# Performance work log

Measured on AMD Instinct MI355X. Metric: run time of the kernel, lower is better.

Reference implementation:

```python
import jax, jax.numpy as jnp
import numpy as np

CH_IN, CH_OUT, KH, KW = 64, 128, 3, 3


def setup_inputs() -> dict:
    key = jax.random.key(0)
    k1, k2, k3 = jax.random.split(key, 3)
    x = jax.random.normal(k1, (16, CH_IN, 256, 256), dtype=jnp.float32)
    W_hat = jax.random.normal(k2, (CH_OUT, CH_IN * KH * KW), dtype=jnp.float32)
    M_hat = jax.random.normal(k3, (CH_OUT, CH_IN * KH * KW), dtype=jnp.float32)
    return {"x": x, "W_hat": W_hat, "M_hat": M_hat}


def reference(x, W_hat, M_hat):
    # NAC weight transform, then a standard same-padded conv (no bias).
    # Patch flattening order in the original (narrow(-1)/narrow(-2) then reshape)
    # matches (C_in, KH, KW) conv weight layout.
    W = jnp.tanh(W_hat) * jax.nn.sigmoid(M_hat)          # [C_out, C_in*KH*KW]
    W = W.reshape(CH_OUT, CH_IN, KH, KW)                  # OIHW
    out = jax.lax.conv_general_dilated(
        x, W,
        window_strides=(1, 1),
        padding=((KH // 2, KH // 2), (KW // 2, KW // 2)),
        dimension_numbers=("NCHW", "OIHW", "NCHW"),
    )
    return out
```

## Files before the change

kernel.cpp:

```cpp
#include <hip/hip_runtime.h>
#include <hip/hip_bf16.h>
#include <stdint.h>


#define CH_IN  64
#define CH_OUT 128
#define HW     256
#define NBATCH 16

typedef __attribute__((ext_vector_type(8))) short short8;
typedef __attribute__((ext_vector_type(4))) float f32x4;

static __device__ __forceinline__ uint32_t pack_bf16(float a, float b) {
    uint32_t ua = __builtin_bit_cast(uint32_t, a);
    uint32_t ub = __builtin_bit_cast(uint32_t, b);
    ua = (ua + 0x7FFFu + ((ua >> 16) & 1u)) >> 16;
    ub = (ub + 0x7FFFu + ((ub >> 16) & 1u));
    return (ua & 0xFFFFu) | (ub & 0xFFFF0000u);
}

__global__ void __launch_bounds__(256) nac_prep(const float* __restrict__ Wh,
                                                const float* __restrict__ Mh,
                                                uint32_t* __restrict__ Af) {
    int f = blockIdx.x * 256 + threadIdx.x;
    if (f >= 9 * 8 * 2 * 64) return;
    int lane = f & 63;
    int s    = (f >> 6) & 1;
    int ms   = (f >> 7) & 7;
    int t    = f >> 10;
    int co   = ms * 16 + (lane & 15);
    int ci0  = s * 32 + ((lane >> 4) << 3);

    uint32_t pk[4];
#pragma unroll
    for (int j2 = 0; j2 < 4; ++j2) {
        int ci = ci0 + 2 * j2;
        int k0 = ci * 9 + t;
        int k1 = k0 + 9;
        float w0 = tanhf(Wh[co * 576 + k0]);
        float m0 = Mh[co * 576 + k0];
        float w1 = tanhf(Wh[co * 576 + k1]);
        float m1 = Mh[co * 576 + k1];
        float v0 = w0 * (1.0f / (1.0f + expf(-m0)));
        float v1 = w1 * (1.0f / (1.0f + expf(-m1)));
        pk[j2] = pack_bf16(v0, v1);
    }
    int fragidx = ((t * 8 + ms) * 2 + s) * 64 + lane;
    reinterpret_cast<uint4*>(Af)[fragidx] = make_uint4(pk[0], pk[1], pk[2], pk[3]);
}

__global__ void __launch_bounds__(256) nac_conv(const float* __restrict__ x,
                                                const uint32_t* __restrict__ Af,
                                                float* __restrict__ out) {
    __shared__ uint32_t xl[8 * 272 * 4];

    unsigned bid = blockIdx.x;
    unsigned idx = (bid & 7u) * 1024u + (bid >> 3);
    int ht = idx & 127;
    int wt = (idx >> 7) & 3;
    int n  = idx >> 9;
    int h0 = ht * 2;
    int w0 = wt * 64;

    int tid = threadIdx.x;

    const float* xn = x + (size_t)n * CH_IN * HW * HW;
    for (int it = 0; it < 9; ++it) {
        int task = tid + it * 256;
        if (task < 2176) {
            int r   = task / 544;
            int rem = task - r * 544;
            int pg  = rem / 68;
            int c   = rem - pg * 68;
            int hrow = h0 - 1 + r;
            int w    = w0 - 1 + c;
            float v[8];
            if ((unsigned)hrow < 256u && (unsigned)w < 256u) {
                const float* p = xn + ((size_t)(pg * 8) * HW + hrow) * HW + w;
#pragma unroll
                for (int e = 0; e < 8; ++e) v[e] = p[(size_t)e * HW * HW];
            } else {
#pragma unroll
                for (int e = 0; e < 8; ++e) v[e] = 0.0f;
            }
            uint4 wd;
            wd.x = pack_bf16(v[0], v[1]);
            wd.y = pack_bf16(v[2], v[3]);
            wd.z = pack_bf16(v[4], v[5]);
            wd.w = pack_bf16(v[6], v[7]);
            *reinterpret_cast<uint4*>(&xl[(pg * 272 + r * 68 + c) * 4]) = wd;
        }
    }
    __syncthreads();

    int lane = tid & 63;
    int wv   = tid >> 6;
    int wm   = wv >> 1;
    int wn   = wv & 1;
    int row4 = lane >> 4;
    int col  = lane & 15;

    f32x4 acc[4][4];
#pragma unroll
    for (int mi = 0; mi < 4; ++mi)
#pragma unroll
        for (int ni = 0; ni < 4; ++ni)
            acc[mi][ni] = (f32x4){0.f, 0.f, 0.f, 0.f};

    const short8* Afr = reinterpret_cast<const short8*>(Af);

    for (int t = 0; t < 9; ++t) {
        int kh = t / 3, kw = t % 3;
        short8 a[2][4];
#pragma unroll
        for (int s = 0; s < 2; ++s)
#pragma unroll
            for (int mi = 0; mi < 4; ++mi)
                a[s][mi] = Afr[((t * 8 + (wm * 4 + mi)) * 2 + s) * 64 + lane];

#pragma unroll
        for (int s = 0; s < 2; ++s) {
            short8 b[4];
#pragma unroll
            for (int ni = 0; ni < 4; ++ni) {
                int pg = s * 4 + row4;
                int pp = (wn + kh) * 68 + ni * 16 + col + kw;
                b[ni] = *reinterpret_cast<const short8*>(&xl[(pg * 272 + pp) * 4]);
            }
#pragma unroll
            for (int mi = 0; mi < 4; ++mi)
#pragma unroll
                for (int ni = 0; ni < 4; ++ni)
                    acc[mi][ni] = __builtin_amdgcn_mfma_f32_16x16x32_bf16(
                        a[s][mi], b[ni], acc[mi][ni], 0, 0, 0);
        }
    }

#pragma unroll
    for (int mi = 0; mi < 4; ++mi) {
#pragma unroll
        for (int reg = 0; reg < 4; ++reg) {
            int co = wm * 64 + mi * 16 + row4 * 4 + reg;
            float* op = out + (((size_t)n * CH_OUT + co) * HW + (h0 + wn)) * HW + w0;
#pragma unroll
            for (int ni = 0; ni < 4; ++ni)
                op[ni * 16 + col] = acc[mi][ni][reg];
        }
    }
}

extern "C" void kernel_launch(void* const* d_in, const int* in_sizes, int n_in,
                              void* d_out, int out_size, void* d_ws, size_t ws_size,
                              hipStream_t stream) {
    const float* x  = (const float*)d_in[0];
    const float* Wh = (const float*)d_in[1];
    const float* Mh = (const float*)d_in[2];
    float* out = (float*)d_out;
    uint32_t* Af = (uint32_t*)d_ws;

    nac_prep<<<36, 256, 0, stream>>>(Wh, Mh, Af);
    nac_conv<<<8192, 256, 0, stream>>>(x, Af, out);
}
```

Measured before the change: 333.0 us.

## Stream 16 output rows per block through a 4-slot LDS ring buffer

```diff
diff --git a/kernel.cpp b/kernel.cpp
--- a/kernel.cpp
+++ b/kernel.cpp
@@ -6,7 +6,6 @@
 #define CH_IN  64
 #define CH_OUT 128
 #define HW     256
-#define NBATCH 16
 
 typedef __attribute__((ext_vector_type(8))) short short8;
 typedef __attribute__((ext_vector_type(4))) float f32x4;
@@ -49,103 +48,152 @@
     reinterpret_cast<uint4*>(Af)[fragidx] = make_uint4(pk[0], pk[1], pk[2], pk[3]);
 }
 
-__global__ void __launch_bounds__(256) nac_conv(const float* __restrict__ x,
-                                                const uint32_t* __restrict__ Af,
-                                                float* __restrict__ out) {
-    __shared__ uint32_t xl[8 * 272 * 4];
+#define NSLOT 4
+#define CW    66
+#define CPAD  69
+#define SLOT_B (CPAD * 16)
+#define PG_B   (NSLOT * CPAD * 16)
+#define S_B    (4 * PG_B)
+
+__global__ void __launch_bounds__(256, 4)
+nac_conv(const float* __restrict__ x, const uint32_t* __restrict__ Af,
+         float* __restrict__ out) {
+    __shared__ uint32_t xl[8 * NSLOT * CPAD * 4];
 
     unsigned bid = blockIdx.x;
-    unsigned idx = (bid & 7u) * 1024u + (bid >> 3);
-    int ht = idx & 127;
-    int wt = (idx >> 7) & 3;
-    int n  = idx >> 9;
-    int h0 = ht * 2;
+    unsigned idx = (bid & 7u) * 128u + (bid >> 3);
+    int ht = idx & 15;
+    int wt = (idx >> 4) & 3;
+    int n  = idx >> 6;
+    int h0 = ht * 16;
     int w0 = wt * 64;
 
-    int tid = threadIdx.x;
+    int tid  = threadIdx.x;
+    int lane = tid & 63;
+    int wm   = tid >> 6;
+    int col  = lane & 15;
+    int row4 = lane >> 4;
 
     const float* xn = x + (size_t)n * CH_IN * HW * HW;
-    for (int it = 0; it < 9; ++it) {
-        int task = tid + it * 256;
-        if (task < 2176) {
-            int r   = task / 544;
-            int rem = task - r * 544;
-            int pg  = rem / 68;
-            int c   = rem - pg * 68;
-            int hrow = h0 - 1 + r;
-            int w    = w0 - 1 + c;
-            float v[8];
-            if ((unsigned)hrow < 256u && (unsigned)w < 256u) {
-                const float* p = xn + ((size_t)(pg * 8) * HW + hrow) * HW + w;
-#pragma unroll
-                for (int e = 0; e < 8; ++e) v[e] = p[(size_t)e * HW * HW];
-            } else {
-#pragma unroll
-                for (int e = 0; e < 8; ++e) v[e] = 0.0f;
+
+    int  pgA  = tid >> 6;
+    int  cA   = tid & 63;
+    bool hasC = tid < 16;
+    int  pgC  = tid >> 1;
+    int  cC   = 64 + (tid & 1);
+    bool wvA  = (unsigned)(w0 - 1 + cA) < (unsigned)HW;
+    bool wvC  = (unsigned)(w0 - 1 + cC) < (unsigned)HW;
+
+    auto issue = [&](int lr, float* xa, float* xb, float* xc) {
+        int hrow = h0 - 1 + lr;
+        bool rv = (unsigned)hrow < (unsigned)HW;
+        bool vA = rv && wvA;
+        bool vC = rv && wvC && hasC;
+        const float* pA = xn + (size_t)hrow * HW + (w0 - 1 + cA);
+        const float* pC = xn + (size_t)hrow * HW + (w0 - 1 + cC);
+        if (vA) {
+#pragma unroll
+            for (int e = 0; e < 8; ++e) {
+                xa[e] = pA[(size_t)(pgA * 8 + e) * HW * HW];
+                xb[e] = pA[(size_t)((pgA + 4) * 8 + e) * HW * HW];
             }
-            uint4 wd;
-            wd.x = pack_bf16(v[0], v[1]);
-            wd.y = pack_bf16(v[2], v[3]);
-            wd.z = pack_bf16(v[4], v[5]);
-            wd.w = pack_bf16(v[6], v[7]);
-            *reinterpret_cast<uint4*>(&xl[(pg * 272 + r * 68 + c) * 4]) = wd;
+        } else {
+#pragma unroll
+            for (int e = 0; e < 8; ++e) { xa[e] = 0.f; xb[e] = 0.f; }
+        }
+        if (vC) {
+#pragma unroll
+            for (int e = 0; e < 8; ++e) xc[e] = pC[(size_t)(pgC * 8 + e) * HW * HW];
+        } else {
+#pragma unroll
+            for (int e = 0; e < 8; ++e) xc[e] = 0.f;
+        }
+    };
+
+    auto commit = [&](int lr, const float* xa, const float* xb, const float* xc) {
+        int slot = lr & 3;
+        uint4 w;
+        w.x = pack_bf16(xa[0], xa[1]); w.y = pack_bf16(xa[2], xa[3]);
+        w.z = pack_bf16(xa[4], xa[5]); w.w = pack_bf16(xa[6], xa[7]);
+        *reinterpret_cast<uint4*>(&xl[((pgA * NSLOT + slot) * CPAD + cA) * 4]) = w;
+        w.x = pack_bf16(xb[0], xb[1]); w.y = pack_bf16(xb[2], xb[3]);
+        w.z = pack_bf16(xb[4], xb[5]); w.w = pack_bf16(xb[6], xb[7]);
+        *reinterpret_cast<uint4*>(&xl[(((pgA + 4) * NSLOT + slot) * CPAD + cA) * 4]) = w;
+        if (hasC) {
+            w.x = pack_bf16(xc[0], xc[1]); w.y = pack_bf16(xc[2], xc[3]);
+            w.z = pack_bf16(xc[4], xc[5]); w.w = pack_bf16(xc[6], xc[7]);
+            *reinterpret_cast<uint4*>(&xl[((pgC * NSLOT + slot) * CPAD + cC) * 4]) = w;
+        }
+    };
+
+    {
+        float xa[8], xb[8], xc[8];
+#pragma unroll
+        for (int lr = 0; lr < 3; ++lr) {
+            issue(lr, xa, xb, xc);
+            commit(lr, xa, xb, xc);
         }
     }
     __syncthreads();
 
-    int lane = tid & 63;
-    int wv   = tid >> 6;
-    int wm   = wv >> 1;
-    int wn   = wv & 1;
-    int row4 = lane >> 4;
-    int col  = lane & 15;
-
-    f32x4 acc[4][4];
-#pragma unroll
-    for (int mi = 0; mi < 4; ++mi)
-#pragma unroll
-        for (int ni = 0; ni < 4; ++ni)
-            acc[mi][ni] = (f32x4){0.f, 0.f, 0.f, 0.f};
+    f32x4 acc[2][4];
+#pragma unroll
+    for (int mi = 0; mi < 2; ++mi)
+#pragma unroll
+        for (int ni = 0; ni < 4; ++ni) acc[mi][ni] = (f32x4){0.f, 0.f, 0.f, 0.f};
 
     const short8* Afr = reinterpret_cast<const short8*>(Af);
-
-    for (int t = 0; t < 9; ++t) {
-        int kh = t / 3, kw = t % 3;
-        short8 a[2][4];
-#pragma unroll
-        for (int s = 0; s < 2; ++s)
-#pragma unroll
-            for (int mi = 0; mi < 4; ++mi)
-                a[s][mi] = Afr[((t * 8 + (wm * 4 + mi)) * 2 + s) * 64 + lane];
-
-#pragma unroll
-        for (int s = 0; s < 2; ++s) {
-            short8 b[4];
-#pragma unroll
-            for (int ni = 0; ni < 4; ++ni) {
-                int pg = s * 4 + row4;
-                int pp = (wn + kh) * 68 + ni * 16 + col + kw;
-                b[ni] = *reinterpret_cast<const short8*>(&xl[(pg * 272 + pp) * 4]);
+    const char* ldsb = reinterpret_cast<const char*>(xl);
+    const int thrbase = row4 * PG_B + col * 16;
+
+    for (int r = 0; r < 16; ++r) {
+        float xa[8], xb[8], xc[8];
+        const bool st = (r < 15);
+        if (st) issue(r + 3, xa, xb, xc);
+
+        int bk0 = thrbase + ((r + 0) & 3) * SLOT_B;
+        int bk1 = thrbase + ((r + 1) & 3) * SLOT_B;
+        int bk2 = thrbase + ((r + 2) & 3) * SLOT_B;
+
+#pragma unroll
+        for (int t = 0; t < 9; ++t) {
+            const int kh = t / 3, kw = t % 3;
+            const int bkh = (kh == 0) ? bk0 : ((kh == 1) ? bk1 : bk2);
+#pragma unroll
+            for (int s = 0; s < 2; ++s) {
+                short8 a0 = Afr[((t * 8 + wm * 2 + 0) * 2 + s) * 64 + lane];
+                short8 a1 = Afr[((t * 8 + wm * 2 + 1) * 2 + s) * 64 + lane];
+#pragma unroll
+                for (int ni = 0; ni < 4; ++ni) {
+                    short8 b = *reinterpret_cast<const short8*>(
+                        ldsb + bkh + s * S_B + (ni * 16 + kw) * 16);
+                    acc[0][ni] = __builtin_amdgcn_mfma_f32_16x16x32_bf16(
+                        a0, b, acc[0][ni], 0, 0, 0);
+                    acc[1][ni] = __builtin_amdgcn_mfma_f32_16x16x32_bf16(
+                        a1, b, acc[1][ni], 0, 0, 0);
+                }
             }
-#pragma unroll
-            for (int mi = 0; mi < 4; ++mi)
-#pragma unroll
-                for (int ni = 0; ni < 4; ++ni)
-                    acc[mi][ni] = __builtin_amdgcn_mfma_f32_16x16x32_bf16(
-                        a[s][mi], b[ni], acc[mi][ni], 0, 0, 0);
-        }
-    }
-
-#pragma unroll
-    for (int mi = 0; mi < 4; ++mi) {
-#pragma unroll
-        for (int reg = 0; reg < 4; ++reg) {
-            int co = wm * 64 + mi * 16 + row4 * 4 + reg;
-            float* op = out + (((size_t)n * CH_OUT + co) * HW + (h0 + wn)) * HW + w0;
-#pragma unroll
-            for (int ni = 0; ni < 4; ++ni)
-                op[ni * 16 + col] = acc[mi][ni][reg];
-        }
+        }
+
+        if (st) {
+            commit(r + 3, xa, xb, xc);
+            __syncthreads();
+        }
+
+        size_t ob = (size_t)n * CH_OUT * HW * HW + (size_t)(h0 + r) * HW + w0;
+#pragma unroll
+        for (int mi = 0; mi < 2; ++mi)
+#pragma unroll
+            for (int reg = 0; reg < 4; ++reg) {
+                int co = wm * 32 + mi * 16 + row4 * 4 + reg;
+                float* op = out + ob + (size_t)co * HW * HW;
+#pragma unroll
+                for (int ni = 0; ni < 4; ++ni) op[ni * 16 + col] = acc[mi][ni][reg];
+            }
+#pragma unroll
+        for (int mi = 0; mi < 2; ++mi)
+#pragma unroll
+            for (int ni = 0; ni < 4; ++ni) acc[mi][ni] = (f32x4){0.f, 0.f, 0.f, 0.f};
     }
 }
 
@@ -159,5 +207,5 @@
     uint32_t* Af = (uint32_t*)d_ws;
 
     nac_prep<<<36, 256, 0, stream>>>(Wh, Mh, Af);
-    nac_conv<<<8192, 256, 0, stream>>>(x, Af, out);
-}
+    nac_conv<<<1024, 256, 0, stream>>>(x, Af, out);
+}
```

New measurement: 563.7 us. 1.69x slower.

## Pre-convert input to NHWC bf16 and stage tiles via direct global-to-LDS loads

Applied to the files above, without the earlier changes.

```diff
diff --git a/kernel.cpp b/kernel.cpp
--- a/kernel.cpp
+++ b/kernel.cpp
@@ -6,10 +6,14 @@
 #define CH_IN  64
 #define CH_OUT 128
 #define HW     256
-#define NBATCH 16
 
 typedef __attribute__((ext_vector_type(8))) short short8;
 typedef __attribute__((ext_vector_type(4))) float f32x4;
+
+#define AF_BYTES 147456u
+#define ZP_BYTE  147456u
+#define XB_BYTE  147712u
+#define WS_NEED  (147712ull + 134217728ull)
 
 static __device__ __forceinline__ uint32_t pack_bf16(float a, float b) {
     uint32_t ua = __builtin_bit_cast(uint32_t, a);
@@ -21,7 +25,9 @@
 
 __global__ void __launch_bounds__(256) nac_prep(const float* __restrict__ Wh,
                                                 const float* __restrict__ Mh,
-                                                uint32_t* __restrict__ Af) {
+                                                uint32_t* __restrict__ ws32) {
+    if (blockIdx.x == 0 && threadIdx.x < 64) ws32[ZP_BYTE / 4 + threadIdx.x] = 0;
+
     int f = blockIdx.x * 256 + threadIdx.x;
     if (f >= 9 * 8 * 2 * 64) return;
     int lane = f & 63;
@@ -46,13 +52,38 @@
         pk[j2] = pack_bf16(v0, v1);
     }
     int fragidx = ((t * 8 + ms) * 2 + s) * 64 + lane;
-    reinterpret_cast<uint4*>(Af)[fragidx] = make_uint4(pk[0], pk[1], pk[2], pk[3]);
-}
-
-__global__ void __launch_bounds__(256) nac_conv(const float* __restrict__ x,
-                                                const uint32_t* __restrict__ Af,
-                                                float* __restrict__ out) {
-    __shared__ uint32_t xl[8 * 272 * 4];
+    reinterpret_cast<uint4*>(ws32)[fragidx] = make_uint4(pk[0], pk[1], pk[2], pk[3]);
+}
+
+__global__ void __launch_bounds__(256) nac_convert(const float* __restrict__ x,
+                                                   uint32_t* __restrict__ xb) {
+    int bid = blockIdx.x;
+    int h   = bid & 255;
+    int n   = bid >> 8;
+    int px  = threadIdx.x;
+    const float* xr = x + ((size_t)n * CH_IN * HW + h) * HW + px;
+    uint32_t* orow = xb + ((size_t)(n * HW + h) * HW + px) * 32;
+#pragma unroll
+    for (int g = 0; g < 8; ++g) {
+        float v0 = xr[(size_t)(g * 8 + 0) * HW * HW];
+        float v1 = xr[(size_t)(g * 8 + 1) * HW * HW];
+        float v2 = xr[(size_t)(g * 8 + 2) * HW * HW];
+        float v3 = xr[(size_t)(g * 8 + 3) * HW * HW];
+        float v4 = xr[(size_t)(g * 8 + 4) * HW * HW];
+        float v5 = xr[(size_t)(g * 8 + 5) * HW * HW];
+        float v6 = xr[(size_t)(g * 8 + 6) * HW * HW];
+        float v7 = xr[(size_t)(g * 8 + 7) * HW * HW];
+        uint4 wd;
+        wd.x = pack_bf16(v0, v1); wd.y = pack_bf16(v2, v3);
+        wd.z = pack_bf16(v4, v5); wd.w = pack_bf16(v6, v7);
+        *reinterpret_cast<uint4*>(orow + g * 4) = wd;
+    }
+}
+
+__global__ void __launch_bounds__(256)
+nac_conv2(const uint32_t* __restrict__ xb, const uint32_t* __restrict__ Af,
+          float* __restrict__ out, const uint32_t* __restrict__ zp) {
+    __shared__ __align__(1024) uint32_t xl[2112 * 4];
 
     unsigned bid = blockIdx.x;
     unsigned idx = (bid & 7u) * 1024u + (bid >> 3);
@@ -62,6 +93,102 @@
     int h0 = ht * 2;
     int w0 = wt * 64;
 
+    int tid = threadIdx.x;
+    int g   = tid & 7;
+    int q   = tid >> 3;
+
+#pragma unroll
+    for (int it = 0; it < 9; ++it) {
+        if (it < 8 || tid < 64) {
+            const int rp = it * 32 + q;
+            const int r0 = (it * 32) / 66;
+            const int r  = (rp >= (r0 + 1) * 66) ? r0 + 1 : r0;
+            const int p  = rp - r * 66;
+            const int hh = h0 - 1 + r;
+            const int ww = w0 - 1 + p;
+            const bool valid = ((unsigned)hh < 256u) & ((unsigned)ww < 256u);
+            const uint32_t* src = valid
+                ? xb + ((size_t)((n * 256 + hh) * 256 + ww) * 32 + ((g ^ (p & 7)) << 2))
+                : zp;
+            __builtin_amdgcn_global_load_lds(
+                (const __attribute__((address_space(1))) uint32_t*)src,
+                (__attribute__((address_space(3))) uint32_t*)&xl[(it * 256 + (tid & ~63)) * 4],
+                16, 0, 0);
+        }
+    }
+    __syncthreads();
+
+    int lane = tid & 63;
+    int wv   = tid >> 6;
+    int wm   = wv >> 1;
+    int wn   = wv & 1;
+    int col  = lane & 15;
+    int row4 = lane >> 4;
+
+    int bcol[2][3];
+#pragma unroll
+    for (int s = 0; s < 2; ++s)
+#pragma unroll
+        for (int kw = 0; kw < 3; ++kw)
+            bcol[s][kw] = (col + kw) * 128 +
+                          ((((s * 4) + row4) ^ ((col + kw) & 7)) * 16);
+
+    f32x4 acc[4][4];
+#pragma unroll
+    for (int mi = 0; mi < 4; ++mi)
+#pragma unroll
+        for (int ni = 0; ni < 4; ++ni) acc[mi][ni] = (f32x4){0.f, 0.f, 0.f, 0.f};
+
+    const short8* Afr = reinterpret_cast<const short8*>(Af);
+    const char* lb = reinterpret_cast<const char*>(xl);
+
+#pragma unroll
+    for (int t = 0; t < 9; ++t) {
+        const int kh = t / 3, kw = t % 3;
+        short8 a[2][4];
+#pragma unroll
+        for (int s = 0; s < 2; ++s)
+#pragma unroll
+            for (int mi = 0; mi < 4; ++mi)
+                a[s][mi] = Afr[((t * 8 + (wm * 4 + mi)) * 2 + s) * 64 + lane];
+#pragma unroll
+        for (int s = 0; s < 2; ++s) {
+#pragma unroll
+            for (int ni = 0; ni < 4; ++ni) {
+                short8 b = *reinterpret_cast<const short8*>(
+                    lb + ((wn + kh) * 66 + ni * 16) * 128 + bcol[s][kw]);
+#pragma unroll
+                for (int mi = 0; mi < 4; ++mi)
+                    acc[mi][ni] = __builtin_amdgcn_mfma_f32_16x16x32_bf16(
+                        a[s][mi], b, acc[mi][ni], 0, 0, 0);
+            }
+        }
+    }
+
+#pragma unroll
+    for (int mi = 0; mi < 4; ++mi) {
+#pragma unroll
+        for (int reg = 0; reg < 4; ++reg) {
+            int co = wm * 64 + mi * 16 + row4 * 4 + reg;
+            float* op = out + (((size_t)n * CH_OUT + co) * HW + (h0 + wn)) * HW + w0;
+#pragma unroll
+            for (int ni = 0; ni < 4; ++ni) op[ni * 16 + col] = acc[mi][ni][reg];
+        }
+    }
+}
+
+__global__ void __launch_bounds__(256) nac_conv_fb(const float* __restrict__ x,
+                                                   const uint32_t* __restrict__ Af,
+                                                   float* __restrict__ out) {
+    __shared__ uint32_t xl[8 * 272 * 4];
+
+    unsigned bid = blockIdx.x;
+    unsigned idx = (bid & 7u) * 1024u + (bid >> 3);
+    int ht = idx & 127;
+    int wt = (idx >> 7) & 3;
+    int n  = idx >> 9;
+    int h0 = ht * 2;
+    int w0 = wt * 64;
     int tid = threadIdx.x;
 
     const float* xn = x + (size_t)n * CH_IN * HW * HW;
@@ -104,11 +231,9 @@
 #pragma unroll
     for (int mi = 0; mi < 4; ++mi)
 #pragma unroll
-        for (int ni = 0; ni < 4; ++ni)
-            acc[mi][ni] = (f32x4){0.f, 0.f, 0.f, 0.f};
+        for (int ni = 0; ni < 4; ++ni) acc[mi][ni] = (f32x4){0.f, 0.f, 0.f, 0.f};
 
     const short8* Afr = reinterpret_cast<const short8*>(Af);
-
     for (int t = 0; t < 9; ++t) {
         int kh = t / 3, kw = t % 3;
         short8 a[2][4];
@@ -117,7 +242,6 @@
 #pragma unroll
             for (int mi = 0; mi < 4; ++mi)
                 a[s][mi] = Afr[((t * 8 + (wm * 4 + mi)) * 2 + s) * 64 + lane];
-
 #pragma unroll
         for (int s = 0; s < 2; ++s) {
             short8 b[4];
@@ -143,8 +267,7 @@
             int co = wm * 64 + mi * 16 + row4 * 4 + reg;
             float* op = out + (((size_t)n * CH_OUT + co) * HW + (h0 + wn)) * HW + w0;
 #pragma unroll
-            for (int ni = 0; ni < 4; ++ni)
-                op[ni * 16 + col] = acc[mi][ni][reg];
+            for (int ni = 0; ni < 4; ++ni) op[ni * 16 + col] = acc[mi][ni][reg];
         }
     }
 }
@@ -156,8 +279,16 @@
     const float* Wh = (const float*)d_in[1];
     const float* Mh = (const float*)d_in[2];
     float* out = (float*)d_out;
-    uint32_t* Af = (uint32_t*)d_ws;
-
-    nac_prep<<<36, 256, 0, stream>>>(Wh, Mh, Af);
-    nac_conv<<<8192, 256, 0, stream>>>(x, Af, out);
-}
+    uint32_t* ws32 = (uint32_t*)d_ws;
+    const uint32_t* Af = ws32;
+    const uint32_t* zp = ws32 + ZP_BYTE / 4;
+    uint32_t* xb = ws32 + XB_BYTE / 4;
+
+    nac_prep<<<36, 256, 0, stream>>>(Wh, Mh, ws32);
+    if (ws_size >= WS_NEED) {
+        nac_convert<<<4096, 256, 0, stream>>>(x, xb);
+        nac_conv2<<<8192, 256, 0, stream>>>(xb, Af, out, zp);
+    } else {
+        nac_conv_fb<<<8192, 256, 0, stream>>>(x, Af, out);
+    }
+}
```

New measurement: 376.7 us. +13.1%, slower.

## Make conv blocks persistent over 32-row strips with rolling LDS row buffer

Applied to the files above, without the earlier changes.

```diff
diff --git a/kernel.cpp b/kernel.cpp
--- a/kernel.cpp
+++ b/kernel.cpp
@@ -6,7 +6,6 @@
 #define CH_IN  64
 #define CH_OUT 128
 #define HW     256
-#define NBATCH 16
 
 typedef __attribute__((ext_vector_type(8))) short short8;
 typedef __attribute__((ext_vector_type(4))) float f32x4;
@@ -17,6 +16,13 @@
     ua = (ua + 0x7FFFu + ((ua >> 16) & 1u)) >> 16;
     ub = (ub + 0x7FFFu + ((ub >> 16) & 1u));
     return (ua & 0xFFFFu) | (ub & 0xFFFF0000u);
+}
+
+static __device__ __forceinline__ uint4 pack8(const float* v) {
+    uint4 w;
+    w.x = pack_bf16(v[0], v[1]); w.y = pack_bf16(v[2], v[3]);
+    w.z = pack_bf16(v[4], v[5]); w.w = pack_bf16(v[6], v[7]);
+    return w;
 }
 
 __global__ void __launch_bounds__(256) nac_prep(const float* __restrict__ Wh,
@@ -49,103 +55,195 @@
     reinterpret_cast<uint4*>(Af)[fragidx] = make_uint4(pk[0], pk[1], pk[2], pk[3]);
 }
 
-__global__ void __launch_bounds__(256) nac_conv(const float* __restrict__ x,
-                                                const uint32_t* __restrict__ Af,
-                                                float* __restrict__ out) {
-    __shared__ uint32_t xl[8 * 272 * 4];
+#define SLOT_B 8448
+
+__global__ void __launch_bounds__(256, 2)
+nac_conv(const float* __restrict__ x, const uint32_t* __restrict__ Af,
+         float* __restrict__ out) {
+    __shared__ __align__(16) uint32_t xl[6 * 528 * 4];
 
     unsigned bid = blockIdx.x;
-    unsigned idx = (bid & 7u) * 1024u + (bid >> 3);
-    int ht = idx & 127;
-    int wt = (idx >> 7) & 3;
-    int n  = idx >> 9;
-    int h0 = ht * 2;
+    unsigned idx = (bid & 7u) * 64u + (bid >> 3);
+    int ht = idx & 7;
+    int wt = (idx >> 3) & 3;
+    int n  = idx >> 5;
+    int h0 = ht * 32;
     int w0 = wt * 64;
 
-    int tid = threadIdx.x;
+    const int tid  = threadIdx.x;
+    const int lane = tid & 63;
+    const int g    = tid & 7;
+    const int ci0  = g * 8;
+    const int wv   = tid >> 6;
+    const int wm   = wv >> 1;
+    const int wn   = wv & 1;
+    const int col  = lane & 15;
+    const int row4 = lane >> 4;
 
     const float* xn = x + (size_t)n * CH_IN * HW * HW;
-    for (int it = 0; it < 9; ++it) {
-        int task = tid + it * 256;
-        if (task < 2176) {
-            int r   = task / 544;
-            int rem = task - r * 544;
-            int pg  = rem / 68;
-            int c   = rem - pg * 68;
-            int hrow = h0 - 1 + r;
-            int w    = w0 - 1 + c;
-            float v[8];
-            if ((unsigned)hrow < 256u && (unsigned)w < 256u) {
-                const float* p = xn + ((size_t)(pg * 8) * HW + hrow) * HW + w;
-#pragma unroll
-                for (int e = 0; e < 8; ++e) v[e] = p[(size_t)e * HW * HW];
-            } else {
-#pragma unroll
-                for (int e = 0; e < 8; ++e) v[e] = 0.0f;
-            }
-            uint4 wd;
-            wd.x = pack_bf16(v[0], v[1]);
-            wd.y = pack_bf16(v[2], v[3]);
-            wd.z = pack_bf16(v[4], v[5]);
-            wd.w = pack_bf16(v[6], v[7]);
-            *reinterpret_cast<uint4*>(&xl[(pg * 272 + r * 68 + c) * 4]) = wd;
+    char* lb = reinterpret_cast<char*>(xl);
+
+    int spx[4], srow[4];
+    spx[0] = tid >> 3;                               srow[0] = 0;
+    spx[1] = 32 + (tid >> 3);                        srow[1] = 0;
+    spx[2] = (tid >= 16) ? ((tid - 16) >> 3) : (64 + (tid >> 3));
+    srow[2] = (tid >= 16) ? 1 : 0;
+    spx[3] = 30 + (tid >> 3);                        srow[3] = 1;
+    const int tpx = 62 + (tid >> 3);
+
+    int dgr[4];
+    int xcol[4];
+    bool wval[4];
+#pragma unroll
+    for (int gi = 0; gi < 4; ++gi) {
+        dgr[gi]  = srow[gi] * 528 + spx[gi] * 8 + (g ^ (spx[gi] & 7));
+        int ww   = w0 - 1 + spx[gi];
+        wval[gi] = (unsigned)ww < 256u;
+        xcol[gi] = wval[gi] ? ww : 0;
+    }
+    const int  tdgr  = 528 + tpx * 8 + (g ^ (tpx & 7));
+    const int  tww   = w0 - 1 + tpx;
+    const bool twval = ((unsigned)tww < 256u) && (tid < 32);
+    const int  txcol = ((unsigned)tww < 256u) ? tww : 0;
+
+    int boff[2][3];
+#pragma unroll
+    for (int s = 0; s < 2; ++s)
+#pragma unroll
+        for (int kw = 0; kw < 3; ++kw) {
+            int p = col + kw;
+            boff[s][kw] = p * 128 + (((s * 4 + row4) ^ (p & 7)) << 4);
+        }
+
+#pragma unroll
+    for (int r = 0; r < 9; ++r) {
+        int j = r * 256 + tid;
+        bool act = (r < 8) || (tid < 64);
+        if (act) {
+            int L  = (j >= 1584) ? 3 : (j >= 1056) ? 2 : (j >= 528) ? 1 : 0;
+            int jr = j - L * 528;
+            int px = jr >> 3;
+            int hh = h0 - 1 + L;
+            int ww = w0 - 1 + px;
+            bool v = ((unsigned)hh < 256u) & ((unsigned)ww < 256u);
+            const float* p = xn + (size_t)ci0 * 65536 +
+                             (size_t)(v ? hh : 0) * 256 + (v ? ww : 0);
+            float sv[8];
+#pragma unroll
+            for (int e = 0; e < 8; ++e) {
+                float val = p[(size_t)e * 65536];
+                sv[e] = v ? val : 0.f;
+            }
+            uint4 wd = pack8(sv);
+            *reinterpret_cast<uint4*>(
+                lb + (L * 528 + px * 8 + (g ^ (px & 7))) * 16) = wd;
         }
     }
     __syncthreads();
 
-    int lane = tid & 63;
-    int wv   = tid >> 6;
-    int wm   = wv >> 1;
-    int wn   = wv & 1;
-    int row4 = lane >> 4;
-    int col  = lane & 15;
-
     f32x4 acc[4][4];
 #pragma unroll
     for (int mi = 0; mi < 4; ++mi)
 #pragma unroll
-        for (int ni = 0; ni < 4; ++ni)
-            acc[mi][ni] = (f32x4){0.f, 0.f, 0.f, 0.f};
-
-    const short8* Afr = reinterpret_cast<const short8*>(Af);
-
-    for (int t = 0; t < 9; ++t) {
-        int kh = t / 3, kw = t % 3;
-        short8 a[2][4];
-#pragma unroll
-        for (int s = 0; s < 2; ++s)
-#pragma unroll
-            for (int mi = 0; mi < 4; ++mi)
-                a[s][mi] = Afr[((t * 8 + (wm * 4 + mi)) * 2 + s) * 64 + lane];
-
-#pragma unroll
-        for (int s = 0; s < 2; ++s) {
-            short8 b[4];
-#pragma unroll
-            for (int ni = 0; ni < 4; ++ni) {
-                int pg = s * 4 + row4;
-                int pp = (wn + kh) * 68 + ni * 16 + col + kw;
-                b[ni] = *reinterpret_cast<const short8*>(&xl[(pg * 272 + pp) * 4]);
-            }
-#pragma unroll
-            for (int mi = 0; mi < 4; ++mi)
-#pragma unroll
-                for (int ni = 0; ni < 4; ++ni)
-                    acc[mi][ni] = __builtin_amdgcn_mfma_f32_16x16x32_bf16(
-                        a[s][mi], b[ni], acc[mi][ni], 0, 0, 0);
-        }
-    }
-
-#pragma unroll
-    for (int mi = 0; mi < 4; ++mi) {
-#pragma unroll
-        for (int reg = 0; reg < 4; ++reg) {
-            int co = wm * 64 + mi * 16 + row4 * 4 + reg;
-            float* op = out + (((size_t)n * CH_OUT + co) * HW + (h0 + wn)) * HW + w0;
-#pragma unroll
-            for (int ni = 0; ni < 4; ++ni)
-                op[ni * 16 + col] = acc[mi][ni][reg];
-        }
+        for (int ni = 0; ni < 4; ++ni) acc[mi][ni] = (f32x4){0.f, 0.f, 0.f, 0.f};
+
+    const short8* Abase = reinterpret_cast<const short8*>(Af) + wm * 512 + lane;
+
+    int slo = wn;
+    int sst = 4;
+
+    for (int c = 0; c < 16; ++c) {
+        const bool st = (c < 15);
+        const int hh0 = h0 + 2 * c + 3;
+
+        float sv[4][8], tv[8];
+        if (st) {
+#pragma unroll
+            for (int gi = 0; gi < 4; ++gi) {
+                int hh = hh0 + srow[gi];
+                bool v = wval[gi] & (hh < 256);
+                const float* p = xn + (size_t)ci0 * 65536 +
+                                 (size_t)(v ? hh : 0) * 256 + xcol[gi];
+#pragma unroll
+                for (int e = 0; e < 8; ++e) {
+                    float val = p[(size_t)e * 65536];
+                    sv[gi][e] = v ? val : 0.f;
+                }
+            }
+            {
+                int hh = hh0 + 1;
+                bool v = twval & (hh < 256);
+                const float* p = xn + (size_t)ci0 * 65536 +
+                                 (size_t)(v ? hh : 0) * 256 + txcol;
+#pragma unroll
+                for (int e = 0; e < 8; ++e) {
+                    float val = p[(size_t)e * 65536];
+                    tv[e] = v ? val : 0.f;
+                }
+            }
+        }
+
+        int sl1 = slo + 1; if (sl1 >= 6) sl1 -= 6;
+        int sl2 = slo + 2; if (sl2 >= 6) sl2 -= 6;
+        const int kb[3] = { slo * SLOT_B, sl1 * SLOT_B, sl2 * SLOT_B };
+
+#pragma unroll
+        for (int t = 0; t < 9; ++t) {
+            const int kh = t / 3, kw = t % 3;
+#pragma unroll
+            for (int s = 0; s < 2; ++s) {
+                short8 a0 = Abase[(t * 16 + 0 * 2 + s) * 64];
+                short8 a1 = Abase[(t * 16 + 1 * 2 + s) * 64];
+                short8 a2 = Abase[(t * 16 + 2 * 2 + s) * 64];
+                short8 a3 = Abase[(t * 16 + 3 * 2 + s) * 64];
+#pragma unroll
+                for (int ni = 0; ni < 4; ++ni) {
+                    short8 b = *reinterpret_cast<const short8*>(
+                        lb + kb[kh] + ni * 2048 + boff[s][kw]);
+                    acc[0][ni] = __builtin_amdgcn_mfma_f32_16x16x32_bf16(
+                        a0, b, acc[0][ni], 0, 0, 0);
+                    acc[1][ni] = __builtin_amdgcn_mfma_f32_16x16x32_bf16(
+                        a1, b, acc[1][ni], 0, 0, 0);
+                    acc[2][ni] = __builtin_amdgcn_mfma_f32_16x16x32_bf16(
+                        a2, b, acc[2][ni], 0, 0, 0);
+                    acc[3][ni] = __builtin_amdgcn_mfma_f32_16x16x32_bf16(
+                        a3, b, acc[3][ni], 0, 0, 0);
+                }
+            }
+        }
+
+        if (st) {
+            const int dbase = sst * SLOT_B;
+#pragma unroll
+            for (int gi = 0; gi < 4; ++gi) {
+                uint4 wd = pack8(sv[gi]);
+                *reinterpret_cast<uint4*>(lb + dbase + dgr[gi] * 16) = wd;
+            }
+            if (tid < 32) {
+                uint4 wd = pack8(tv);
+                *reinterpret_cast<uint4*>(lb + dbase + tdgr * 16) = wd;
+            }
+        }
+        __syncthreads();
+
+        const int rr = h0 + 2 * c + wn;
+        const size_t ob = (size_t)n * CH_OUT * 65536 + (size_t)rr * 256 + w0;
+#pragma unroll
+        for (int mi = 0; mi < 4; ++mi)
+#pragma unroll
+            for (int reg = 0; reg < 4; ++reg) {
+                int co = wm * 64 + mi * 16 + row4 * 4 + reg;
+                float* op = out + ob + (size_t)co * 65536;
+#pragma unroll
+                for (int ni = 0; ni < 4; ++ni) op[ni * 16 + col] = acc[mi][ni][reg];
+            }
+#pragma unroll
+        for (int mi = 0; mi < 4; ++mi)
+#pragma unroll
+            for (int ni = 0; ni < 4; ++ni) acc[mi][ni] = (f32x4){0.f, 0.f, 0.f, 0.f};
+
+        slo += 2; if (slo >= 6) slo -= 6;
+        sst += 2; if (sst >= 6) sst -= 6;
     }
 }
 
@@ -159,5 +257,5 @@
     uint32_t* Af = (uint32_t*)d_ws;
 
     nac_prep<<<36, 256, 0, stream>>>(Wh, Mh, Af);
-    nac_conv<<<8192, 256, 0, stream>>>(x, Af, out);
-}
+    nac_conv<<<512, 256, 0, stream>>>(x, Af, out);
+}
```

Result: slower. 740.0 us (+122.2%).
